# Optimization experiments

Measured on AMD Instinct MI355X. Metric: run time of the kernel, lower is better.

## Reference

```python
import jax, jax.numpy as jnp
import numpy as np

B, S, I, H = 512, 1024, 20, 64  # batch, seq_len, input_size, hidden_size


def setup_inputs() -> dict:
    key = jax.random.key(0)
    ks = jax.random.split(key, 12)
    # one-hot protein sequences with variable true lengths (padding is all-zero rows)
    lengths = jax.random.randint(ks[0], (B,), 100, S + 1)
    tokens = jax.random.randint(ks[1], (B, S), 0, I)
    valid = (jnp.arange(S)[None, :] < lengths[:, None]).astype(jnp.float32)
    input1 = jax.nn.one_hot(tokens, I, dtype=jnp.float32) * valid[:, :, None]

    def nrm(k, shape, s=0.05):
        return jax.random.normal(k, shape, jnp.float32) * s

    return {
        'input1': input1,
        'W_ih_f': nrm(ks[2], (4 * H, I)), 'W_hh_f': nrm(ks[3], (4 * H, H)), 'b_f': nrm(ks[4], (4 * H,)),
        'W_ih_b': nrm(ks[5], (4 * H, I)), 'W_hh_b': nrm(ks[6], (4 * H, H)), 'b_b': nrm(ks[7], (4 * H,)),
        'conv1_w': nrm(ks[8], (20, 20), 1.0),           # blosum pssm: [out_c=20, kernel_w=20]
        'conv2_w': nrm(ks[9], (100, 4, 20)), 'conv2_b': nrm(ks[9], (100,)),
        'fc1_w': nrm(ks[10], (64, 228)), 'fc1_b': nrm(ks[10], (64,)),
        'fc2_w': nrm(ks[11], (2, 64)), 'fc2_b': nrm(ks[11], (2,)),
    }


def _lstm_final(x, W_ih, W_hh, b):
    # x: [B,S,I] -> final hidden state [B,H]; torch gate order i,f,g,o
    xs = jnp.einsum('bsi,gi->sbg', x, W_ih) + b  # [S,B,4H]

    def step(carry, gx):
        h, c = carry
        g = gx + h @ W_hh.T
        i, f, gg, o = jnp.split(g, 4, axis=-1)
        c = jax.nn.sigmoid(f) * c + jax.nn.sigmoid(i) * jnp.tanh(gg)
        h = jax.nn.sigmoid(o) * jnp.tanh(c)
        return (h, c), None

    init = (jnp.zeros((x.shape[0], H), x.dtype), jnp.zeros((x.shape[0], H), x.dtype))
    (h, _), _ = jax.lax.scan(step, init, xs)
    return h


def reference(input1, W_ih_f, W_hh_f, b_f, W_ih_b, W_hh_b, b_b,
              conv1_w, conv2_w, conv2_b, fc1_w, fc1_b, fc2_w, fc2_b):
    # BiLSTM: final hidden state of each direction (dropout is identity in eval)
    h_fw = _lstm_final(input1, W_ih_f, W_hh_f, b_f)
    h_bw = _lstm_final(input1[:, ::-1, :], W_ih_b, W_hh_b, b_b)
    lstm_output = jnp.concatenate([h_fw, h_bw], axis=1)  # [B,128]

    # conv1: kernel (1,20) spans the full width -> per-position linear map. [B,20,S]
    c1 = jnp.einsum('bsj,cj->bcs', input1, conv1_w)
    # faithful torch.reshape (B,20,S,1)->(B,S,1,20): row-major reinterpretation
    c1 = c1.reshape(input1.shape[0], S, 20)  # [B,S,20]

    # ragged 4-bin segment mean over the first width[i]=4*(len[i]//4) positions
    lens = jnp.sum(input1, axis=(1, 2)).astype(jnp.int32)
    bw = jnp.floor(lens / 4).astype(jnp.int32)
    width = bw * 4
    pos = jnp.arange(S)[None, :]                       # [1,S]
    bin_idx = pos // bw[:, None]                       # [B,S]
    valid = pos < width[:, None]                       # [B,S]
    mask = ((bin_idx[:, None, :] == jnp.arange(4)[None, :, None]) & valid[:, None, :]).astype(c1.dtype)  # [B,4,S]
    avblock = jnp.einsum('bks,bsc->bkc', mask, c1) / bw.astype(c1.dtype)[:, None, None]  # [B,4,20]

    # conv2: kernel (4,20) spans the whole avblock -> one dot per out channel
    c2 = jnp.einsum('bkc,okc->bo', avblock, conv2_w) + conv2_b  # [B,100]
    c2 = jax.nn.relu(c2)

    merged = jnp.concatenate([lstm_output, c2], axis=1)  # [B,228]
    fc1 = merged @ fc1_w.T + fc1_b
    fc2 = fc1 @ fc2_w.T + fc2_b
    return jax.nn.softmax(fc2, axis=1)
```

## Files before the change

kernel.cpp:

```cpp
#include <hip/hip_runtime.h>
#include <hip/hip_bf16.h>

#define BB 512
#define SS 1024
#define NI 20
#define HH 64
#define NG 256
#define MB4 4
#define PAD 80
#define TROW 260

typedef unsigned short u16;
typedef unsigned int u32;
typedef unsigned long long u64;
typedef _Float16 f16;
typedef f16 f16x8 __attribute__((ext_vector_type(8)));
typedef float f32x4 __attribute__((ext_vector_type(4)));

#define LOG2E 1.4426950408889634f

__device__ __forceinline__ float bf2f(u16 b) { return __uint_as_float(((u32)b) << 16); }
__device__ __forceinline__ float ldw(const void* p, int idx, int mode) {
  return mode ? bf2f(((const u16*)p)[idx]) : ((const float*)p)[idx];
}
__device__ __forceinline__ float frcp(float x) { return __builtin_amdgcn_rcpf(x); }
__device__ __forceinline__ float fexp2(float x) { return __builtin_amdgcn_exp2f(x); }

union __align__(16) SharedU {
  struct __align__(16) {
    float table[21 * TROW];
    f16 hbuf[2][MB4][PAD];
    short tok_s[SS * MB4];
  } l;
  struct __align__(16) {
    u32 stg[5120];
    float c1w[400];
    short tok_c[SS];
    int redc[256];
    float pav[3][80];
    float avg[80];
    float cpart[2][100];
  } c;
};

__global__ __launch_bounds__(256)
void lstm_kernel(const void* in1,
                 const void* Wih_f, const void* Whh_f, const void* b_f,
                 const void* Wih_b, const void* Whh_b, const void* b_b,
                 const void* conv1_w, const void* conv2_w, const void* conv2_b,
                 float* hout, float* c2g) {
  int bx = blockIdx.x;
  int t = threadIdx.x;

  __shared__ SharedU sh;
  __shared__ int mode_sh;

  if (t == 0) mode_sh = 1;
  __syncthreads();
  {
    float v = bf2f(((const u16*)b_f)[t]);
    if (!(fabsf(v) < 1000.0f)) atomicAnd(&mode_sh, 0);
  }
  __syncthreads();
  int mode = mode_sh;

  if (bx < 256) {
    auto& L = sh.l;
    int dir = bx >> 7;
    int b0 = (bx & 127) * MB4;
    int w = t >> 6, lane = t & 63, l = lane & 15, q = lane >> 4;
    int bsel = l >> 2;
    const void* Wih = dir ? Wih_b : Wih_f;
    const void* Whh = dir ? Whh_b : Whh_f;
    const void* bv  = dir ? b_b   : b_f;

    for (int m = 0; m < MB4; ++m) {
      if (mode) {
        u32* st = (u32*)L.table;
        for (int k0 = 0; k0 < 4; ++k0) {
          const u32* src = (const u32*)in1 + ((size_t)(b0 + m) * SS + k0 * 256) * 10;
#pragma unroll
          for (int i = 0; i < 10; ++i) st[t + i * 256] = src[t + i * 256];
          __syncthreads();
          const u32* row = st + t * 10;
          int tok = -1;
#pragma unroll
          for (int ww = 0; ww < 10; ++ww) {
            u32 u = row[ww];
            if (u & 0xFFFFu) tok = 2 * ww;
            if (u >> 16)     tok = 2 * ww + 1;
          }
          L.tok_s[(k0 * 256 + t) * MB4 + m] = (short)(tok + 1);
          __syncthreads();
        }
      } else {
        float4* st = (float4*)L.table;
        for (int k0 = 0; k0 < 4; ++k0) {
          const float4* src = (const float4*)((const float*)in1 + ((size_t)(b0 + m) * SS + k0 * 256) * 20);
#pragma unroll
          for (int i = 0; i < 5; ++i) st[t + i * 256] = src[t + i * 256];
          __syncthreads();
          const float* row = (const float*)L.table + t * 20;
          int tok = -1;
#pragma unroll
          for (int ww = 0; ww < 20; ++ww)
            if (row[ww] != 0.f) tok = ww;
          L.tok_s[(k0 * 256 + t) * MB4 + m] = (short)(tok + 1);
          __syncthreads();
        }
      }
    }

    for (int idx = t; idx < 21 * 256; idx += 256) {
      int r = idx >> 8, g = idx & 255;
      float scl = ((g >> 6) == 2) ? (2.f * LOG2E) : (-LOG2E);
      float v = ldw(bv, g, mode);
      if (r > 0) v += ldw(Wih, g * NI + (r - 1), mode);
      L.table[r * TROW + (g & 63) * 4 + (g >> 6)] = scl * v;
    }
    f16x8 Bf[4][2];
#pragma unroll
    for (int tt = 0; tt < 4; ++tt) {
      float scl = (tt == 2) ? (2.f * LOG2E) : (-LOG2E);
      int g = 64 * tt + 16 * w + l;
#pragma unroll
      for (int kc = 0; kc < 2; ++kc) {
        f16x8 v;
#pragma unroll
        for (int j = 0; j < 8; ++j)
          v[j] = (f16)(scl * ldw(Whh, g * HH + kc * 32 + q * 8 + j, mode));
        Bf[tt][kc] = v;
      }
    }
    for (int idx = t; idx < 2 * MB4 * PAD; idx += 256)
      ((f16*)L.hbuf)[idx] = (f16)0.f;
    __syncthreads();

    float d_st = 0.f, hlast = 0.f;
    int jj = 16 * w + l;

    f32x4 wxc;
    {
      int pos0 = dir ? (SS - 1) : 0;
      wxc = *(const f32x4*)&L.table[(int)L.tok_s[pos0 * MB4 + q] * TROW + jj * 4];
    }
    int tok1;
    {
      int pos1 = dir ? (SS - 2) : 1;
      tok1 = (int)L.tok_s[pos1 * MB4 + q];
    }

    const f32x4 Z = {0.f, 0.f, 0.f, 0.f};

#pragma unroll 2
    for (int s = 0; s < SS; ++s) {
      int p = s & 1;
      f16x8 a0 = *(const f16x8*)&L.hbuf[p][bsel][q * 8];
      f16x8 a1 = *(const f16x8*)&L.hbuf[p][bsel][32 + q * 8];
      f32x4 wxn = *(const f32x4*)&L.table[tok1 * TROW + jj * 4];
      {
        int pos2 = (dir ? (SS - 3 - s) : (s + 2)) & (SS - 1);
        tok1 = (int)L.tok_s[pos2 * MB4 + q];
      }

      f32x4 accA[4], accB[4];
#pragma unroll
      for (int tt = 0; tt < 4; ++tt)
        accA[tt] = __builtin_amdgcn_mfma_f32_16x16x32_f16(a0, Bf[tt][0], Z, 0, 0, 0);
#pragma unroll
      for (int tt = 0; tt < 4; ++tt)
        accB[tt] = __builtin_amdgcn_mfma_f32_16x16x32_f16(a1, Bf[tt][1], Z, 0, 0, 0);

      float g_i = accA[0][0] + accB[0][0] + wxc[0];
      float g_f = accA[1][0] + accB[1][0] + wxc[1];
      float g_g = accA[2][0] + accB[2][0] + wxc[2];
      float g_o = accA[3][0] + accB[3][0] + wxc[3];

      {
        float Ei = fexp2(g_i);
        float Ef = fexp2(g_f);
        float G  = fexp2(g_g);
        float Eo = fexp2(g_o);
        float F   = frcp(Ef + 1.f);
        float Itg = (G - 1.f) * frcp((Ei + 1.f) * (G + 1.f));
        float dnew = fmaf(F, d_st, (2.f * LOG2E) * Itg);
        d_st = dnew;
        float C = fexp2(dnew);
        float hv = (C - 1.f) * frcp((Eo + 1.f) * (C + 1.f));
        hlast = hv;
        L.hbuf[p ^ 1][q][jj] = (f16)hv;
      }
      __syncthreads();
      wxc = wxn;
    }
    hout[(b0 + q) * 128 + dir * 64 + jj] = hlast;

  } else {
    auto& C = sh.c;
    int b = bx - 256;
    int cnt = 0;
    if (mode) {
      for (int k0 = 0; k0 < 4; ++k0) {
        const u32* src = (const u32*)in1 + ((size_t)b * SS + k0 * 256) * 10;
#pragma unroll
        for (int i = 0; i < 10; ++i) C.stg[t + i * 256] = src[t + i * 256];
        __syncthreads();
        const u32* row = C.stg + t * 10;
        int tok = -1;
#pragma unroll
        for (int ww = 0; ww < 10; ++ww) {
          u32 u = row[ww];
          if (u & 0xFFFFu) tok = 2 * ww;
          if (u >> 16)     tok = 2 * ww + 1;
        }
        C.tok_c[k0 * 256 + t] = (short)tok;
        cnt += (tok >= 0);
        __syncthreads();
      }
    } else {
      float4* st = (float4*)C.stg;
      for (int k0 = 0; k0 < 4; ++k0) {
        const float4* src = (const float4*)((const float*)in1 + ((size_t)b * SS + k0 * 256) * 20);
#pragma unroll
        for (int i = 0; i < 5; ++i) st[t + i * 256] = src[t + i * 256];
        __syncthreads();
        const float* row = (const float*)C.stg + t * 20;
        int tok = -1;
#pragma unroll
        for (int ww = 0; ww < 20; ++ww)
          if (row[ww] != 0.f) tok = ww;
        C.tok_c[k0 * 256 + t] = (short)tok;
        cnt += (tok >= 0);
        __syncthreads();
      }
    }
    C.redc[t] = cnt;
    __syncthreads();
    for (int stp = 128; stp > 0; stp >>= 1) {
      if (t < stp) C.redc[t] += C.redc[t + stp];
      __syncthreads();
    }
    int len = C.redc[0];
    int bw = len >> 2;

    for (int i = t; i < 400; i += 256) C.c1w[i] = ldw(conv1_w, i, mode);
    __syncthreads();

    if (t < 240) {
      int seg = t / 80;
      int u = t - seg * 80;
      int k = u / 20, cc = u % 20;
      int base = k * bw;
      int s0 = base + (seg * bw) / 3;
      int s1 = base + ((seg + 1) * bw) / 3;
      float p0 = 0.f, p1 = 0.f, p2 = 0.f, p3 = 0.f;
      int s = s0;
      for (; s + 4 <= s1; s += 4) {
        int f0 = s * 20 + cc, f1 = f0 + 20, f2 = f0 + 40, f3 = f0 + 60;
        int tk0 = C.tok_c[f0 & 1023];
        int tk1 = C.tok_c[f1 & 1023];
        int tk2 = C.tok_c[f2 & 1023];
        int tk3 = C.tok_c[f3 & 1023];
        if (tk0 >= 0) p0 += C.c1w[(f0 >> 10) * 20 + tk0];
        if (tk1 >= 0) p1 += C.c1w[(f1 >> 10) * 20 + tk1];
        if (tk2 >= 0) p2 += C.c1w[(f2 >> 10) * 20 + tk2];
        if (tk3 >= 0) p3 += C.c1w[(f3 >> 10) * 20 + tk3];
      }
      for (; s < s1; ++s) {
        int f = s * 20 + cc;
        int tk = C.tok_c[f & 1023];
        if (tk >= 0) p0 += C.c1w[(f >> 10) * 20 + tk];
      }
      C.pav[seg][u] = (p0 + p1) + (p2 + p3);
    }
    __syncthreads();
    if (t < 80) C.avg[t] = (C.pav[0][t] + C.pav[1][t] + C.pav[2][t]) / (float)bw;
    __syncthreads();

    if (t < 200) {
      int half = t / 100, o = t - half * 100;
      float dot = 0.f;
      int q0 = half * 40;
#pragma unroll 8
      for (int q = q0; q < q0 + 40; ++q)
        dot = fmaf(C.avg[q], ldw(conv2_w, o * 80 + q, mode), dot);
      C.cpart[half][o] = dot;
    }
    __syncthreads();
    if (t < 100) {
      float dot = C.cpart[0][t] + C.cpart[1][t] + ldw(conv2_b, t, mode);
      c2g[b * 100 + t] = dot > 0.f ? dot : 0.f;
    }
  }
}

__global__ __launch_bounds__(256)
void head_kernel(const void* fc1_w, const void* fc1_b,
                 const void* fc2_w, const void* fc2_b,
                 const void* bvec, const float* hout, const float* c2g, void* out) {
  int b = blockIdx.x;
  int t = threadIdx.x;
  __shared__ float merged[228];
  __shared__ float fpart[4][64];
  __shared__ float fc1v[64];
  __shared__ float f2p[2][64];
  __shared__ int mode_sh;

  if (t == 0) mode_sh = 1;
  __syncthreads();
  {
    float v = bf2f(((const u16*)bvec)[t]);
    if (!(fabsf(v) < 1000.0f)) atomicAnd(&mode_sh, 0);
  }
  __syncthreads();
  int mode = mode_sh;

  if (t < 128) merged[t] = hout[b * 128 + t];
  else if (t < 228) merged[t] = c2g[b * 100 + (t - 128)];
  __syncthreads();

  {
    int o = t & 63, ch = t >> 6;
    float v = 0.f;
    int m0 = ch * 57;
#pragma unroll 8
    for (int m = m0; m < m0 + 57; ++m)
      v = fmaf(merged[m], ldw(fc1_w, o * 228 + m, mode), v);
    fpart[ch][o] = v;
  }
  __syncthreads();
  if (t < 64)
    fc1v[t] = fpart[0][t] + fpart[1][t] + fpart[2][t] + fpart[3][t] + ldw(fc1_b, t, mode);
  __syncthreads();

  if (t < 128) {
    int o = t >> 6, m = t & 63;
    f2p[o][m] = fc1v[m] * ldw(fc2_w, o * 64 + m, mode);
  }
  __syncthreads();
  for (int stp = 32; stp > 0; stp >>= 1) {
    if (t < 128) {
      int o = t >> 6, m = t & 63;
      if (m < stp) f2p[o][m] += f2p[o][m + stp];
    }
    __syncthreads();
  }
  if (t == 0) {
    float x0 = f2p[0][0] + ldw(fc2_b, 0, mode);
    float x1 = f2p[1][0] + ldw(fc2_b, 1, mode);
    float mx = fmaxf(x0, x1);
    float e0 = fexp2(LOG2E * (x0 - mx)), e1 = fexp2(LOG2E * (x1 - mx));
    float inv = frcp(e0 + e1);
    if (mode) {
      ((__hip_bfloat16*)out)[b * 2 + 0] = __float2bfloat16(e0 * inv);
      ((__hip_bfloat16*)out)[b * 2 + 1] = __float2bfloat16(e1 * inv);
    } else {
      ((float*)out)[b * 2 + 0] = e0 * inv;
      ((float*)out)[b * 2 + 1] = e1 * inv;
    }
  }
}

extern "C" void kernel_launch(void* const* d_in, const int* in_sizes, int n_in,
                              void* d_out, int out_size, void* d_ws, size_t ws_size,
                              hipStream_t stream) {
  (void)in_sizes; (void)n_in; (void)out_size; (void)ws_size;
  char* ws = (char*)d_ws;
  float* hout = (float*)(ws + 256);
  float* c2g  = (float*)(ws + 256 + (size_t)BB * 128 * 4);

  lstm_kernel<<<768, 256, 0, stream>>>(d_in[0],
                                       d_in[1], d_in[2], d_in[3],
                                       d_in[4], d_in[5], d_in[6],
                                       d_in[7], d_in[8], d_in[9],
                                       hout, c2g);
  head_kernel<<<BB, 256, 0, stream>>>(d_in[10], d_in[11], d_in[12], d_in[13],
                                      d_in[3], hout, c2g, d_out);
}
```

Baseline: 370.6 us.

## Fuse head MLP into conv blocks using flag-based wait on LSTM blocks

Removes the separate head kernel launch. Each conv block now computes conv2 locally, spin-waits on per-group release flags set by the forward and backward LSTM blocks, then runs fc1/fc2/softmax in place. This saves one kernel launch and the c2g global round trip, but adds a memset launch and relies on the LSTM blocks being co-resident or scheduled ahead of the spinning conv blocks to avoid deadlock.

```diff
diff --git a/kernel.cpp b/kernel.cpp
--- a/kernel.cpp
+++ b/kernel.cpp
@@ -40,6 +40,11 @@
     float pav[3][80];
     float avg[80];
     float cpart[2][100];
+    float c2loc[100];
+    float merged[228];
+    float fpart[4][64];
+    float fc1v[64];
+    float f2p[2][64];
   } c;
 };
 
@@ -48,7 +53,9 @@
                  const void* Wih_f, const void* Whh_f, const void* b_f,
                  const void* Wih_b, const void* Whh_b, const void* b_b,
                  const void* conv1_w, const void* conv2_w, const void* conv2_b,
-                 float* hout, float* c2g) {
+                 const void* fc1_w, const void* fc1_b,
+                 const void* fc2_w, const void* fc2_b,
+                 int* flags, float* hout, void* out) {
   int bx = blockIdx.x;
   int t = threadIdx.x;
 
@@ -194,6 +201,12 @@
       wxc = wxn;
     }
     hout[(b0 + q) * 128 + dir * 64 + jj] = hlast;
+
+    __threadfence();
+    __syncthreads();
+    if (t == 0)
+      __hip_atomic_store(&flags[dir * 128 + (bx & 127)], 1,
+                         __ATOMIC_RELEASE, __HIP_MEMORY_SCOPE_AGENT);
 
   } else {
     auto& C = sh.c;
@@ -289,74 +302,64 @@
     __syncthreads();
     if (t < 100) {
       float dot = C.cpart[0][t] + C.cpart[1][t] + ldw(conv2_b, t, mode);
-      c2g[b * 100 + t] = dot > 0.f ? dot : 0.f;
-    }
-  }
-}
-
-__global__ __launch_bounds__(256)
-void head_kernel(const void* fc1_w, const void* fc1_b,
-                 const void* fc2_w, const void* fc2_b,
-                 const void* bvec, const float* hout, const float* c2g, void* out) {
-  int b = blockIdx.x;
-  int t = threadIdx.x;
-  __shared__ float merged[228];
-  __shared__ float fpart[4][64];
-  __shared__ float fc1v[64];
-  __shared__ float f2p[2][64];
-  __shared__ int mode_sh;
-
-  if (t == 0) mode_sh = 1;
-  __syncthreads();
-  {
-    float v = bf2f(((const u16*)bvec)[t]);
-    if (!(fabsf(v) < 1000.0f)) atomicAnd(&mode_sh, 0);
-  }
-  __syncthreads();
-  int mode = mode_sh;
-
-  if (t < 128) merged[t] = hout[b * 128 + t];
-  else if (t < 228) merged[t] = c2g[b * 100 + (t - 128)];
-  __syncthreads();
-
-  {
-    int o = t & 63, ch = t >> 6;
-    float v = 0.f;
-    int m0 = ch * 57;
+      C.c2loc[t] = dot > 0.f ? dot : 0.f;
+    }
+
+    int grp = b >> 2;
+    if (t == 0) {
+      for (;;) {
+        int fa = __hip_atomic_load(&flags[grp],       __ATOMIC_ACQUIRE, __HIP_MEMORY_SCOPE_AGENT);
+        int fb = __hip_atomic_load(&flags[128 + grp], __ATOMIC_ACQUIRE, __HIP_MEMORY_SCOPE_AGENT);
+        if (fa && fb) break;
+        __builtin_amdgcn_s_sleep(32);
+      }
+    }
+    __syncthreads();
+    __threadfence();
+
+    if (t < 128) C.merged[t] = hout[b * 128 + t];
+    else if (t < 228) C.merged[t] = C.c2loc[t - 128];
+    __syncthreads();
+
+    {
+      int o = t & 63, ch = t >> 6;
+      float v = 0.f;
+      int m0 = ch * 57;
 #pragma unroll 8
-    for (int m = m0; m < m0 + 57; ++m)
-      v = fmaf(merged[m], ldw(fc1_w, o * 228 + m, mode), v);
-    fpart[ch][o] = v;
-  }
-  __syncthreads();
-  if (t < 64)
-    fc1v[t] = fpart[0][t] + fpart[1][t] + fpart[2][t] + fpart[3][t] + ldw(fc1_b, t, mode);
-  __syncthreads();
-
-  if (t < 128) {
-    int o = t >> 6, m = t & 63;
-    f2p[o][m] = fc1v[m] * ldw(fc2_w, o * 64 + m, mode);
-  }
-  __syncthreads();
-  for (int stp = 32; stp > 0; stp >>= 1) {
+      for (int m = m0; m < m0 + 57; ++m)
+        v = fmaf(C.merged[m], ldw(fc1_w, o * 228 + m, mode), v);
+      C.fpart[ch][o] = v;
+    }
+    __syncthreads();
+    if (t < 64)
+      C.fc1v[t] = C.fpart[0][t] + C.fpart[1][t] + C.fpart[2][t] + C.fpart[3][t] + ldw(fc1_b, t, mode);
+    __syncthreads();
+
     if (t < 128) {
       int o = t >> 6, m = t & 63;
-      if (m < stp) f2p[o][m] += f2p[o][m + stp];
-    }
-    __syncthreads();
-  }
-  if (t == 0) {
-    float x0 = f2p[0][0] + ldw(fc2_b, 0, mode);
-    float x1 = f2p[1][0] + ldw(fc2_b, 1, mode);
-    float mx = fmaxf(x0, x1);
-    float e0 = fexp2(LOG2E * (x0 - mx)), e1 = fexp2(LOG2E * (x1 - mx));
-    float inv = frcp(e0 + e1);
-    if (mode) {
-      ((__hip_bfloat16*)out)[b * 2 + 0] = __float2bfloat16(e0 * inv);
-      ((__hip_bfloat16*)out)[b * 2 + 1] = __float2bfloat16(e1 * inv);
-    } else {
-      ((float*)out)[b * 2 + 0] = e0 * inv;
-      ((float*)out)[b * 2 + 1] = e1 * inv;
+      C.f2p[o][m] = C.fc1v[m] * ldw(fc2_w, o * 64 + m, mode);
+    }
+    __syncthreads();
+    for (int stp = 32; stp > 0; stp >>= 1) {
+      if (t < 128) {
+        int o = t >> 6, m = t & 63;
+        if (m < stp) C.f2p[o][m] += C.f2p[o][m + stp];
+      }
+      __syncthreads();
+    }
+    if (t == 0) {
+      float x0 = C.f2p[0][0] + ldw(fc2_b, 0, mode);
+      float x1 = C.f2p[1][0] + ldw(fc2_b, 1, mode);
+      float mx = fmaxf(x0, x1);
+      float e0 = fexp2(LOG2E * (x0 - mx)), e1 = fexp2(LOG2E * (x1 - mx));
+      float inv = frcp(e0 + e1);
+      if (mode) {
+        ((__hip_bfloat16*)out)[b * 2 + 0] = __float2bfloat16(e0 * inv);
+        ((__hip_bfloat16*)out)[b * 2 + 1] = __float2bfloat16(e1 * inv);
+      } else {
+        ((float*)out)[b * 2 + 0] = e0 * inv;
+        ((float*)out)[b * 2 + 1] = e1 * inv;
+      }
     }
   }
 }
@@ -366,14 +369,14 @@
                               hipStream_t stream) {
   (void)in_sizes; (void)n_in; (void)out_size; (void)ws_size;
   char* ws = (char*)d_ws;
-  float* hout = (float*)(ws + 256);
-  float* c2g  = (float*)(ws + 256 + (size_t)BB * 128 * 4);
-
+  int*   flags = (int*)ws;
+  float* hout  = (float*)(ws + 1024);
+
+  hipMemsetAsync(flags, 0, 1024, stream);
   lstm_kernel<<<768, 256, 0, stream>>>(d_in[0],
                                        d_in[1], d_in[2], d_in[3],
                                        d_in[4], d_in[5], d_in[6],
                                        d_in[7], d_in[8], d_in[9],
-                                       hout, c2g);
-  head_kernel<<<BB, 256, 0, stream>>>(d_in[10], d_in[11], d_in[12], d_in[13],
-                                      d_in[3], hout, c2g, d_out);
+                                       d_in[10], d_in[11], d_in[12], d_in[13],
+                                       flags, hout, d_out);
 }
```

After: 494.0 us. 1.33x slower.

## Run LSTM recurrence in a single wavefront to remove per-step block barriers

Applied to the files above, without the earlier changes.

The LSTM recurrence now runs on one wavefront per block instead of four. That wave holds all 16 gate tiles of W_hh in registers and computes all 64 hidden units for the 4 batch rows. This removes the __syncthreads on every timestep and replaces the double-buffered hidden state with a single LDS buffer. The cost is four times the MFMA and activation work per wave on the serial critical path, and more register pressure from 32 f16x8 weight fragments.

```diff
diff --git a/kernel.cpp b/kernel.cpp
--- a/kernel.cpp
+++ b/kernel.cpp
@@ -29,7 +29,7 @@
 union __align__(16) SharedU {
   struct __align__(16) {
     float table[21 * TROW];
-    f16 hbuf[2][MB4][PAD];
+    f16 h[MB4 * PAD];
     short tok_s[SS * MB4];
   } l;
   struct __align__(16) {
@@ -69,7 +69,6 @@
     int dir = bx >> 7;
     int b0 = (bx & 127) * MB4;
     int w = t >> 6, lane = t & 63, l = lane & 15, q = lane >> 4;
-    int bsel = l >> 2;
     const void* Wih = dir ? Wih_b : Wih_f;
     const void* Whh = dir ? Whh_b : Whh_f;
     const void* bv  = dir ? b_b   : b_f;
@@ -118,82 +117,86 @@
       if (r > 0) v += ldw(Wih, g * NI + (r - 1), mode);
       L.table[r * TROW + (g & 63) * 4 + (g >> 6)] = scl * v;
     }
-    f16x8 Bf[4][2];
-#pragma unroll
-    for (int tt = 0; tt < 4; ++tt) {
-      float scl = (tt == 2) ? (2.f * LOG2E) : (-LOG2E);
-      int g = 64 * tt + 16 * w + l;
+    __syncthreads();
+    if (w != 0) return;
+
+    f16x8 Bf[16][2];
+#pragma unroll
+    for (int T = 0; T < 16; ++T) {
+      float scl = ((T >> 2) == 2) ? (2.f * LOG2E) : (-LOG2E);
+      int g = 16 * T + l;
 #pragma unroll
       for (int kc = 0; kc < 2; ++kc) {
         f16x8 v;
 #pragma unroll
         for (int j = 0; j < 8; ++j)
           v[j] = (f16)(scl * ldw(Whh, g * HH + kc * 32 + q * 8 + j, mode));
-        Bf[tt][kc] = v;
-      }
-    }
-    for (int idx = t; idx < 2 * MB4 * PAD; idx += 256)
-      ((f16*)L.hbuf)[idx] = (f16)0.f;
-    __syncthreads();
-
-    float d_st = 0.f, hlast = 0.f;
-    int jj = 16 * w + l;
-
-    f32x4 wxc;
+        Bf[T][kc] = v;
+      }
+    }
+    f16* h16 = L.h;
+    for (int i = lane; i < MB4 * PAD; i += 64) h16[i] = (f16)0.f;
+
+    int bsel = l >> 2;
+    float d_st0 = 0.f, d_st1 = 0.f, d_st2 = 0.f, d_st3 = 0.f;
+    float hl0 = 0.f, hl1 = 0.f, hl2 = 0.f, hl3 = 0.f;
+
+    int tokc, tok1;
     {
       int pos0 = dir ? (SS - 1) : 0;
-      wxc = *(const f32x4*)&L.table[(int)L.tok_s[pos0 * MB4 + q] * TROW + jj * 4];
-    }
-    int tok1;
-    {
       int pos1 = dir ? (SS - 2) : 1;
+      tokc = (int)L.tok_s[pos0 * MB4 + q];
       tok1 = (int)L.tok_s[pos1 * MB4 + q];
     }
-
     const f32x4 Z = {0.f, 0.f, 0.f, 0.f};
 
-#pragma unroll 2
+#pragma unroll 1
     for (int s = 0; s < SS; ++s) {
-      int p = s & 1;
-      f16x8 a0 = *(const f16x8*)&L.hbuf[p][bsel][q * 8];
-      f16x8 a1 = *(const f16x8*)&L.hbuf[p][bsel][32 + q * 8];
-      f32x4 wxn = *(const f32x4*)&L.table[tok1 * TROW + jj * 4];
+      f16x8 a0 = *(const f16x8*)&h16[bsel * PAD + 8 * q];
+      f16x8 a1 = *(const f16x8*)&h16[bsel * PAD + 32 + 8 * q];
+      f32x4 wx0 = *(const f32x4*)&L.table[tokc * TROW + (0 * 16 + l) * 4];
+      f32x4 wx1 = *(const f32x4*)&L.table[tokc * TROW + (1 * 16 + l) * 4];
+      f32x4 wx2 = *(const f32x4*)&L.table[tokc * TROW + (2 * 16 + l) * 4];
+      f32x4 wx3 = *(const f32x4*)&L.table[tokc * TROW + (3 * 16 + l) * 4];
       {
         int pos2 = (dir ? (SS - 3 - s) : (s + 2)) & (SS - 1);
+        tokc = tok1;
         tok1 = (int)L.tok_s[pos2 * MB4 + q];
       }
 
-      f32x4 accA[4], accB[4];
-#pragma unroll
-      for (int tt = 0; tt < 4; ++tt)
-        accA[tt] = __builtin_amdgcn_mfma_f32_16x16x32_f16(a0, Bf[tt][0], Z, 0, 0, 0);
-#pragma unroll
-      for (int tt = 0; tt < 4; ++tt)
-        accB[tt] = __builtin_amdgcn_mfma_f32_16x16x32_f16(a1, Bf[tt][1], Z, 0, 0, 0);
-
-      float g_i = accA[0][0] + accB[0][0] + wxc[0];
-      float g_f = accA[1][0] + accB[1][0] + wxc[1];
-      float g_g = accA[2][0] + accB[2][0] + wxc[2];
-      float g_o = accA[3][0] + accB[3][0] + wxc[3];
-
-      {
-        float Ei = fexp2(g_i);
-        float Ef = fexp2(g_f);
-        float G  = fexp2(g_g);
-        float Eo = fexp2(g_o);
-        float F   = frcp(Ef + 1.f);
-        float Itg = (G - 1.f) * frcp((Ei + 1.f) * (G + 1.f));
-        float dnew = fmaf(F, d_st, (2.f * LOG2E) * Itg);
-        d_st = dnew;
-        float C = fexp2(dnew);
-        float hv = (C - 1.f) * frcp((Eo + 1.f) * (C + 1.f));
-        hlast = hv;
-        L.hbuf[p ^ 1][q][jj] = (f16)hv;
-      }
-      __syncthreads();
-      wxc = wxn;
-    }
-    hout[(b0 + q) * 128 + dir * 64 + jj] = hlast;
+      float gv[16];
+#pragma unroll
+      for (int T = 0; T < 16; ++T) {
+        f32x4 acc = __builtin_amdgcn_mfma_f32_16x16x32_f16(a0, Bf[T][0], Z, 0, 0, 0);
+        acc = __builtin_amdgcn_mfma_f32_16x16x32_f16(a1, Bf[T][1], acc, 0, 0, 0);
+        gv[T] = acc[0];
+      }
+
+#define ACT(c, wxv, dst, hlv)                                            \
+      {                                                                  \
+        float Ei = fexp2(gv[c] + wxv[0]);                                \
+        float Ef = fexp2(gv[4 + c] + wxv[1]);                            \
+        float G  = fexp2(gv[8 + c] + wxv[2]);                            \
+        float Eo = fexp2(gv[12 + c] + wxv[3]);                           \
+        float F   = frcp(Ef + 1.f);                                      \
+        float Itg = (G - 1.f) * frcp((Ei + 1.f) * (G + 1.f));            \
+        float dnew = fmaf(F, dst, (2.f * LOG2E) * Itg);                  \
+        dst = dnew;                                                      \
+        float C = fexp2(dnew);                                           \
+        float hv = (C - 1.f) * frcp((Eo + 1.f) * (C + 1.f));             \
+        hlv = hv;                                                        \
+        h16[q * PAD + c * 16 + l] = (f16)hv;                             \
+      }
+      ACT(0, wx0, d_st0, hl0)
+      ACT(1, wx1, d_st1, hl1)
+      ACT(2, wx2, d_st2, hl2)
+      ACT(3, wx3, d_st3, hl3)
+#undef ACT
+    }
+    hout[(b0 + q) * 128 + dir * 64 +  0 + l] = hl0;
+    hout[(b0 + q) * 128 + dir * 64 + 16 + l] = hl1;
+    hout[(b0 + q) * 128 + dir * 64 + 32 + l] = hl2;
+    hout[(b0 + q) * 128 + dir * 64 + 48 + l] = hl3;
 
   } else {
     auto& C = sh.c;
```

After: 699.0 us. 1.89x slower.
